# Optimization experiments

Measured on AMD Instinct MI355X. Metric: run time of the kernel, lower is better.

Reference implementation:

```python
import jax, jax.numpy as jnp
import numpy as np

N_EMBEDDINGS = 1024
EMBEDDING_DIM = 256
DECAY = 0.99
EPSILON = 1e-05


def setup_inputs() -> dict:
    key = jax.random.key(0)
    k1, k2, k3 = jax.random.split(key, 3)
    inputs = jax.random.normal(k1, (16, 64, 64, EMBEDDING_DIM), dtype=jnp.float32)
    codebook = jax.random.normal(k2, (N_EMBEDDINGS, EMBEDDING_DIM), dtype=jnp.float32)
    ema_w = jax.random.normal(k3, (N_EMBEDDINGS, EMBEDDING_DIM), dtype=jnp.float32)
    ema_cluster_size = jnp.zeros((N_EMBEDDINGS,), dtype=jnp.float32)
    return {"inputs": inputs, "codebook": codebook, "ema_w": ema_w,
            "ema_cluster_size": ema_cluster_size}


def reference(inputs, codebook, ema_w, ema_cluster_size):
    input_shape = inputs.shape
    flat = inputs.reshape(-1, EMBEDDING_DIM)  # [N, D]
    # Squared Euclidean pairwise distances: [N, K]
    dists = (jnp.sum(flat * flat, axis=1, keepdims=True)
             + jnp.sum(codebook * codebook, axis=1)[None, :]
             - 2.0 * flat @ codebook.T)
    idx = jnp.argmin(dists, axis=1)  # [N]
    encodings = jax.nn.one_hot(idx, N_EMBEDDINGS, dtype=flat.dtype)  # [N, K]
    quantized = (encodings @ codebook).reshape(input_shape)
    # EMA updates (training mode)
    cs = ema_cluster_size * DECAY + (1.0 - DECAY) * jnp.sum(encodings, axis=0)
    n = jnp.sum(cs)
    cs = (cs + EPSILON) / (n + cs * EPSILON) * n  # faithful to original expression
    dw = encodings.T @ flat  # [K, D] scatter-accumulate via matmul
    new_ema_w = ema_w * DECAY + (1.0 - DECAY) * dw
    new_codebook = new_ema_w / cs[:, None]
    return quantized, encodings, cs, new_ema_w, new_codebook
```

## Files before the change

### kernel.cpp

```cpp
#include <hip/hip_runtime.h>

#define N_ROWS 65536
#define D 256
#define K 1024
#define DECAYF 0.99f
#define OMDF 0.01f
#define EPSF 1e-5f

typedef _Float16 f16;
typedef _Float16 f16x8 __attribute__((ext_vector_type(8)));
typedef float f32x16 __attribute__((ext_vector_type(16)));

__global__ __launch_bounds__(256) void prep_kernel(const float* __restrict__ cb,
                                                   float* __restrict__ cnorm,
                                                   char* __restrict__ wsB,
                                                   float* __restrict__ dw,
                                                   float* __restrict__ counts) {
    const int tid = threadIdx.x;
    const int bid = blockIdx.x;
    const int g = bid * 256 + tid;
    *reinterpret_cast<float4*>(dw + (size_t)g * 4) = make_float4(0.f, 0.f, 0.f, 0.f);
    if (g < K) counts[g] = 0.f;
    {
        const int row = bid * 4 + (tid >> 6);
        const int lane = tid & 63;
        const float4 v = *reinterpret_cast<const float4*>(cb + (size_t)row * D + lane * 4);
        float s = v.x * v.x + v.y * v.y + v.z * v.z + v.w * v.w;
        #pragma unroll
        for (int m = 32; m; m >>= 1) s += __shfl_xor(s, m);
        if (lane == 0) cnorm[row] = s;
    }
    {
        const int sp = g & 15;
        const int c = (g >> 4) & 255;
        const int sd = g >> 12;
        const int ct = sd >> 2, dk = sd & 3;
        const int sl = sp ^ (c & 7);
        const int v = sl >> 3, ks = (sl >> 1) & 3, h = sl & 1;
        const float* src = cb + (size_t)(ct * 256 + c) * D + dk * 64 + ks * 16 + h * 8;
        f16 out[8];
        #pragma unroll
        for (int e = 0; e < 8; ++e) {
            const float f = src[e];
            const f16 hi = (f16)f;
            out[e] = v ? (f16)(f - (float)hi) : hi;
        }
        *reinterpret_cast<f16x8*>(wsB + (size_t)g * 16) = *reinterpret_cast<f16x8*>(out);
    }
}

__global__ __launch_bounds__(256, 2) void argmin_mfma_kernel(
        const float* __restrict__ x, const float* __restrict__ cb,
        const char* __restrict__ wsB, const float* __restrict__ cnorm,
        int* __restrict__ idx_out, float* __restrict__ counts,
        float* __restrict__ quant, float* __restrict__ enc) {
    __shared__ char smem[81920];
    char* Alds = smem;
    char* Blds = smem + 16384;
    const int tid = threadIdx.x;
    const int wave = tid >> 6;
    const int lane = tid & 63;
    const int rw = wave >> 1;
    const int cw = wave & 1;
    const int l31 = lane & 31;
    const int h = lane >> 5;
    const int n0 = blockIdx.x * 64;

    float bestv[16];
    int besti[16];
    #pragma unroll
    for (int r = 0; r < 16; ++r) { bestv[r] = 3.4e38f; besti[r] = 0; }

    const int s_row = tid >> 2;
    const int s_c4 = tid & 3;

    for (int ct = 0; ct < 4; ++ct) {
        f32x16 acc[4];
        #pragma unroll
        for (int cf = 0; cf < 4; ++cf)
            #pragma unroll
            for (int r = 0; r < 16; ++r) acc[cf][r] = 0.f;

        for (int dks = 0; dks < 4; ++dks) {
            const int dk = (ct & 1) ? (3 - dks) : dks;
            __syncthreads();
            if (!(ct > 0 && dks == 0)) {
                const float4* xs = reinterpret_cast<const float4*>(
                    x + (size_t)(n0 + s_row) * D + dk * 64 + s_c4 * 16);
                float f[16];
                {
                    const float4 f0 = xs[0], f1 = xs[1], f2 = xs[2], f3 = xs[3];
                    f[0]=f0.x; f[1]=f0.y; f[2]=f0.z; f[3]=f0.w;
                    f[4]=f1.x; f[5]=f1.y; f[6]=f1.z; f[7]=f1.w;
                    f[8]=f2.x; f[9]=f2.y; f[10]=f2.z; f[11]=f2.w;
                    f[12]=f3.x; f[13]=f3.y; f[14]=f3.z; f[15]=f3.w;
                }
                f16 hi[16], lo[16];
                #pragma unroll
                for (int e = 0; e < 16; ++e) {
                    hi[e] = (f16)f[e];
                    lo[e] = (f16)(f[e] - (float)hi[e]);
                }
                const int sw = s_row & 7;
                char* Abase = Alds + s_row * 256;
                *reinterpret_cast<f16x8*>(Abase + (((s_c4 * 2 + 0) ^ sw) * 16)) = *reinterpret_cast<f16x8*>(&hi[0]);
                *reinterpret_cast<f16x8*>(Abase + (((s_c4 * 2 + 1) ^ sw) * 16)) = *reinterpret_cast<f16x8*>(&hi[8]);
                *reinterpret_cast<f16x8*>(Abase + (((8 + s_c4 * 2 + 0) ^ sw) * 16)) = *reinterpret_cast<f16x8*>(&lo[0]);
                *reinterpret_cast<f16x8*>(Abase + (((8 + s_c4 * 2 + 1) ^ sw) * 16)) = *reinterpret_cast<f16x8*>(&lo[8]);
            }
            {
                const int4* gsrc = reinterpret_cast<const int4*>(wsB + ((size_t)(ct * 4 + dk) << 16));
                int4* ldst = reinterpret_cast<int4*>(Blds);
                #pragma unroll
                for (int i = 0; i < 16; ++i) ldst[tid + i * 256] = gsrc[tid + i * 256];
            }
            __syncthreads();
            const int arow = rw * 32 + l31;
            const int asw = arow & 7;
            #pragma unroll
            for (int ks = 0; ks < 4; ++ks) {
                const int sA = ks * 2 + h;
                const f16x8 Ah = *reinterpret_cast<const f16x8*>(Alds + arow * 256 + ((sA ^ asw) * 16));
                const f16x8 Al = *reinterpret_cast<const f16x8*>(Alds + arow * 256 + (((8 + sA) ^ asw) * 16));
                #pragma unroll
                for (int cf = 0; cf < 4; ++cf) {
                    const int bcode = cw * 128 + cf * 32 + l31;
                    const char* Bbase = Blds + bcode * 256;
                    const int bsw = bcode & 7;
                    const f16x8 Bh = *reinterpret_cast<const f16x8*>(Bbase + ((sA ^ bsw) * 16));
                    const f16x8 Bl = *reinterpret_cast<const f16x8*>(Bbase + (((8 + sA) ^ bsw) * 16));
                    acc[cf] = __builtin_amdgcn_mfma_f32_32x32x16_f16(Ah, Bh, acc[cf], 0, 0, 0);
                    acc[cf] = __builtin_amdgcn_mfma_f32_32x32x16_f16(Ah, Bl, acc[cf], 0, 0, 0);
                    acc[cf] = __builtin_amdgcn_mfma_f32_32x32x16_f16(Al, Bh, acc[cf], 0, 0, 0);
                }
            }
        }
        #pragma unroll
        for (int cf = 0; cf < 4; ++cf) {
            const int code = ct * 256 + cw * 128 + cf * 32 + l31;
            const float cn = cnorm[code];
            #pragma unroll
            for (int r = 0; r < 16; ++r) {
                const float dist = cn - 2.f * acc[cf][r];
                if (dist < bestv[r]) { bestv[r] = dist; besti[r] = code; }
            }
        }
    }
    #pragma unroll
    for (int r = 0; r < 16; ++r) {
        float v = bestv[r];
        int b = besti[r];
        #pragma unroll
        for (int m = 16; m; m >>= 1) {
            const float ov = __shfl_xor(v, m);
            const int ob = __shfl_xor(b, m);
            if (ov < v || (ov == v && ob < b)) { v = ov; b = ob; }
        }
        bestv[r] = v; besti[r] = b;
    }
    __syncthreads();
    float* Sv = reinterpret_cast<float*>(smem);
    int*   Si = reinterpret_cast<int*>(smem + 512);
    if (l31 == 0) {
        #pragma unroll
        for (int r = 0; r < 16; ++r) {
            const int row = rw * 32 + (r & 3) + 8 * (r >> 2) + 4 * h;
            Sv[cw * 64 + row] = bestv[r];
            Si[cw * 64 + row] = besti[r];
        }
    }
    __syncthreads();
    if (tid < 64) {
        const float v0 = Sv[tid], v1 = Sv[64 + tid];
        const int b0 = Si[tid], b1 = Si[64 + tid];
        const bool take1 = (v1 < v0) || (v1 == v0 && b1 < b0);
        const int b = take1 ? b1 : b0;
        idx_out[n0 + tid] = b;
        atomicAdd(&counts[b], 1.0f);
        Si[tid] = b;
    }
    __syncthreads();
    {
        const int k0 = tid * 4;
        #pragma unroll 4
        for (int r = 0; r < 64; ++r) {
            const int ir = Si[r];
            float4 v;
            v.x = (k0 == ir) ? 1.f : 0.f;
            v.y = (k0 + 1 == ir) ? 1.f : 0.f;
            v.z = (k0 + 2 == ir) ? 1.f : 0.f;
            v.w = (k0 + 3 == ir) ? 1.f : 0.f;
            *reinterpret_cast<float4*>(enc + (((size_t)(n0 + r)) << 10) + k0) = v;
        }
    }
    #pragma unroll
    for (int it = 0; it < 16; ++it) {
        const int r = it * 4 + wave;
        const int ir = Si[r];
        const float4 c = *reinterpret_cast<const float4*>(cb + (size_t)ir * D + lane * 4);
        *reinterpret_cast<float4*>(quant + (size_t)(n0 + r) * D + lane * 4) = c;
    }
}

__global__ __launch_bounds__(1024) void cs_scan_kernel(const float* __restrict__ ema_cs,
                                                       const float* __restrict__ counts,
                                                       float* __restrict__ cs_out,
                                                       int* __restrict__ cursor) {
    __shared__ float wsum[16];
    __shared__ int wisum[16];
    __shared__ float n_sh;
    const int k = threadIdx.x;
    const int wid = k >> 6;
    const int lane = k & 63;
    const float cnt = counts[k];
    const float c = ema_cs[k] * DECAYF + OMDF * cnt;
    const int ic = (int)cnt;
    int v = ic;
    #pragma unroll
    for (int d = 1; d < 64; d <<= 1) {
        const int t = __shfl_up(v, d);
        if (lane >= d) v += t;
    }
    float s = c;
    #pragma unroll
    for (int m = 32; m; m >>= 1) s += __shfl_xor(s, m);
    if (lane == 63) wisum[wid] = v;
    if (lane == 0) wsum[wid] = s;
    __syncthreads();
    if (k == 0) {
        float n = 0.f;
        for (int w = 0; w < 16; ++w) n += wsum[w];
        n_sh = n;
    }
    if (wid == 0 && lane < 16) {
        int wv = wisum[lane];
        #pragma unroll
        for (int d = 1; d < 16; d <<= 1) {
            const int t = __shfl_up(wv, d);
            if (lane >= d) wv += t;
        }
        wisum[lane] = wv;
    }
    __syncthreads();
    const float n = n_sh;
    cs_out[k] = (c + EPSF) / (n + c * EPSF) * n;
    const int wbase = (wid == 0) ? 0 : wisum[wid - 1];
    cursor[k] = wbase + v - ic;
}

__global__ __launch_bounds__(256) void scatter_kernel(const int* __restrict__ idx,
                                                      int* __restrict__ cursor,
                                                      int* __restrict__ rowlist,
                                                      int* __restrict__ codelist) {
    const int n = blockIdx.x * 256 + threadIdx.x;
    const int i = idx[n];
    const int pos = atomicAdd(&cursor[i], 1);
    rowlist[pos] = n;
    codelist[pos] = i;
}

__global__ __launch_bounds__(256) void chunk_sum_kernel(const float* __restrict__ x,
                                                        const int* __restrict__ rowlist,
                                                        const int* __restrict__ codelist,
                                                        float* __restrict__ dw) {
    const int wave = threadIdx.x >> 6;
    const int lane = threadIdx.x & 63;
    const int p0 = blockIdx.x * 32 + wave * 8;
    int rows[8], codes[8];
    #pragma unroll
    for (int j = 0; j < 8; ++j) {
        rows[j] = rowlist[p0 + j];
        codes[j] = codelist[p0 + j];
    }
    float4 v[8];
    #pragma unroll
    for (int j = 0; j < 8; ++j)
        v[j] = *reinterpret_cast<const float4*>(x + (size_t)rows[j] * D + lane * 4);
    float4 s = v[0];
    int cur = codes[0];
    #pragma unroll
    for (int j = 1; j < 8; ++j) {
        if (codes[j] != cur) {
            float* dst = dw + (size_t)cur * D + lane * 4;
            atomicAdd(dst + 0, s.x); atomicAdd(dst + 1, s.y);
            atomicAdd(dst + 2, s.z); atomicAdd(dst + 3, s.w);
            cur = codes[j];
            s = v[j];
        } else {
            s.x += v[j].x; s.y += v[j].y; s.z += v[j].z; s.w += v[j].w;
        }
    }
    float* dst = dw + (size_t)cur * D + lane * 4;
    atomicAdd(dst + 0, s.x); atomicAdd(dst + 1, s.y);
    atomicAdd(dst + 2, s.z); atomicAdd(dst + 3, s.w);
}

__global__ __launch_bounds__(256) void ema_kernel(const float* __restrict__ ema_w,
                                                  const float* __restrict__ dw,
                                                  const float* __restrict__ cs,
                                                  float* __restrict__ w_out,
                                                  float* __restrict__ cb_out) {
    const int e4 = blockIdx.x * blockDim.x + threadIdx.x;
    const int k = e4 >> 6;
    const float csk = cs[k];
    const float4 w = *reinterpret_cast<const float4*>(ema_w + (size_t)e4 * 4);
    const float4 d = *reinterpret_cast<const float4*>(dw + (size_t)e4 * 4);
    float4 nw, nc;
    nw.x = w.x * DECAYF + OMDF * d.x;
    nw.y = w.y * DECAYF + OMDF * d.y;
    nw.z = w.z * DECAYF + OMDF * d.z;
    nw.w = w.w * DECAYF + OMDF * d.w;
    nc.x = nw.x / csk; nc.y = nw.y / csk; nc.z = nw.z / csk; nc.w = nw.w / csk;
    *reinterpret_cast<float4*>(w_out + (size_t)e4 * 4) = nw;
    *reinterpret_cast<float4*>(cb_out + (size_t)e4 * 4) = nc;
}

extern "C" void kernel_launch(void* const* d_in, const int* in_sizes, int n_in,
                              void* d_out, int out_size, void* d_ws, size_t ws_size,
                              hipStream_t stream) {
    (void)in_sizes; (void)n_in; (void)out_size; (void)ws_size;
    const float* x      = (const float*)d_in[0];
    const float* cb     = (const float*)d_in[1];
    const float* ema_w  = (const float*)d_in[2];
    const float* ema_cs = (const float*)d_in[3];

    float* out    = (float*)d_out;
    float* quant  = out;
    float* enc    = quant + 16777216;
    float* cs_out = enc + 67108864;
    float* w_out  = cs_out + 1024;
    float* cb_out = w_out + 262144;

    float* ws       = (float*)d_ws;
    float* counts   = ws;
    float* dw       = ws + 1024;
    float* cnorm    = ws + 263168;
    int*   cursor   = (int*)(ws + 264192);
    int*   idx      = (int*)(ws + 265216);
    int*   rowlist  = (int*)(ws + 330752);
    int*   codelist = (int*)(ws + 396288);
    char*  wsB      = (char*)(ws + 461824);

    prep_kernel<<<256, 256, 0, stream>>>(cb, cnorm, wsB, dw, counts);
    argmin_mfma_kernel<<<N_ROWS / 64, 256, 0, stream>>>(x, cb, wsB, cnorm, idx, counts,
                                                        quant, enc);
    cs_scan_kernel<<<1, 1024, 0, stream>>>(ema_cs, counts, cs_out, cursor);
    scatter_kernel<<<N_ROWS / 256, 256, 0, stream>>>(idx, cursor, rowlist, codelist);
    chunk_sum_kernel<<<2048, 256, 0, stream>>>(x, rowlist, codelist, dw);
    ema_kernel<<<65536 / 256, 256, 0, stream>>>(ema_w, dw, cs_out, w_out, cb_out);
}
```

Before: 347.5 us.

## Split one-hot and quantized writes into separate nontemporal kernels, widen LDS swizzle

Moves writing the 256MB one-hot encoding matrix and the quantized output out of the MFMA argmin kernel into two dedicated streaming kernels that use nontemporal stores. The aim is to stop the compute kernel from stalling on the large write tail and to let the writes run at full bandwidth across the whole GPU. It also widens the LDS XOR swizzle from 8 to 16 slots to reduce bank conflicts. The split adds two kernel launches, and the new kernels must re-read the index array.

```diff
diff --git a/kernel.cpp b/kernel.cpp
--- a/kernel.cpp
+++ b/kernel.cpp
@@ -10,6 +10,7 @@
 typedef _Float16 f16;
 typedef _Float16 f16x8 __attribute__((ext_vector_type(8)));
 typedef float f32x16 __attribute__((ext_vector_type(16)));
+typedef float f32x4 __attribute__((ext_vector_type(4)));
 
 __global__ __launch_bounds__(256) void prep_kernel(const float* __restrict__ cb,
                                                    float* __restrict__ cnorm,
@@ -35,7 +36,7 @@
         const int c = (g >> 4) & 255;
         const int sd = g >> 12;
         const int ct = sd >> 2, dk = sd & 3;
-        const int sl = sp ^ (c & 7);
+        const int sl = sp ^ (c & 15);
         const int v = sl >> 3, ks = (sl >> 1) & 3, h = sl & 1;
         const float* src = cb + (size_t)(ct * 256 + c) * D + dk * 64 + ks * 16 + h * 8;
         f16 out[8];
@@ -50,10 +51,9 @@
 }
 
 __global__ __launch_bounds__(256, 2) void argmin_mfma_kernel(
-        const float* __restrict__ x, const float* __restrict__ cb,
-        const char* __restrict__ wsB, const float* __restrict__ cnorm,
-        int* __restrict__ idx_out, float* __restrict__ counts,
-        float* __restrict__ quant, float* __restrict__ enc) {
+        const float* __restrict__ x, const char* __restrict__ wsB,
+        const float* __restrict__ cnorm, int* __restrict__ idx_out,
+        float* __restrict__ counts) {
     __shared__ char smem[81920];
     char* Alds = smem;
     char* Blds = smem + 16384;
@@ -101,7 +101,7 @@
                     hi[e] = (f16)f[e];
                     lo[e] = (f16)(f[e] - (float)hi[e]);
                 }
-                const int sw = s_row & 7;
+                const int sw = s_row & 15;
                 char* Abase = Alds + s_row * 256;
                 *reinterpret_cast<f16x8*>(Abase + (((s_c4 * 2 + 0) ^ sw) * 16)) = *reinterpret_cast<f16x8*>(&hi[0]);
                 *reinterpret_cast<f16x8*>(Abase + (((s_c4 * 2 + 1) ^ sw) * 16)) = *reinterpret_cast<f16x8*>(&hi[8]);
@@ -116,7 +116,7 @@
             }
             __syncthreads();
             const int arow = rw * 32 + l31;
-            const int asw = arow & 7;
+            const int asw = arow & 15;
             #pragma unroll
             for (int ks = 0; ks < 4; ++ks) {
                 const int sA = ks * 2 + h;
@@ -126,7 +126,7 @@
                 for (int cf = 0; cf < 4; ++cf) {
                     const int bcode = cw * 128 + cf * 32 + l31;
                     const char* Bbase = Blds + bcode * 256;
-                    const int bsw = bcode & 7;
+                    const int bsw = bcode & 15;
                     const f16x8 Bh = *reinterpret_cast<const f16x8*>(Bbase + ((sA ^ bsw) * 16));
                     const f16x8 Bl = *reinterpret_cast<const f16x8*>(Bbase + (((8 + sA) ^ bsw) * 16));
                     acc[cf] = __builtin_amdgcn_mfma_f32_32x32x16_f16(Ah, Bh, acc[cf], 0, 0, 0);
@@ -177,28 +177,33 @@
         const int b = take1 ? b1 : b0;
         idx_out[n0 + tid] = b;
         atomicAdd(&counts[b], 1.0f);
-        Si[tid] = b;
-    }
-    __syncthreads();
-    {
-        const int k0 = tid * 4;
-        #pragma unroll 4
-        for (int r = 0; r < 64; ++r) {
-            const int ir = Si[r];
-            float4 v;
-            v.x = (k0 == ir) ? 1.f : 0.f;
-            v.y = (k0 + 1 == ir) ? 1.f : 0.f;
-            v.z = (k0 + 2 == ir) ? 1.f : 0.f;
-            v.w = (k0 + 3 == ir) ? 1.f : 0.f;
-            *reinterpret_cast<float4*>(enc + (((size_t)(n0 + r)) << 10) + k0) = v;
-        }
-    }
-    #pragma unroll
-    for (int it = 0; it < 16; ++it) {
-        const int r = it * 4 + wave;
-        const int ir = Si[r];
-        const float4 c = *reinterpret_cast<const float4*>(cb + (size_t)ir * D + lane * 4);
-        *reinterpret_cast<float4*>(quant + (size_t)(n0 + r) * D + lane * 4) = c;
+    }
+}
+
+__global__ __launch_bounds__(256) void quant_kernel(const float* __restrict__ cb,
+                                                    const int* __restrict__ idx,
+                                                    float* __restrict__ quant) {
+    const int n = blockIdx.x * 4 + (threadIdx.x >> 6);
+    const int lane = threadIdx.x & 63;
+    const int i = idx[n];
+    const f32x4 c = *reinterpret_cast<const f32x4*>(cb + (size_t)i * D + lane * 4);
+    __builtin_nontemporal_store(c, reinterpret_cast<f32x4*>(quant + (size_t)n * D + lane * 4));
+}
+
+__global__ __launch_bounds__(256) void enc_kernel(const int* __restrict__ idx,
+                                                  float* __restrict__ enc) {
+    const int total = N_ROWS * (K / 4);
+    for (int g = blockIdx.x * blockDim.x + threadIdx.x; g < total;
+         g += gridDim.x * blockDim.x) {
+        const int n = g >> 8;
+        const int k0 = (g & 255) * 4;
+        const int i = idx[n];
+        f32x4 v;
+        v[0] = (k0 == i) ? 1.f : 0.f;
+        v[1] = (k0 + 1 == i) ? 1.f : 0.f;
+        v[2] = (k0 + 2 == i) ? 1.f : 0.f;
+        v[3] = (k0 + 3 == i) ? 1.f : 0.f;
+        __builtin_nontemporal_store(v, reinterpret_cast<f32x4*>(enc + (size_t)g * 4));
     }
 }
 
@@ -342,8 +347,9 @@
     char*  wsB      = (char*)(ws + 461824);
 
     prep_kernel<<<256, 256, 0, stream>>>(cb, cnorm, wsB, dw, counts);
-    argmin_mfma_kernel<<<N_ROWS / 64, 256, 0, stream>>>(x, cb, wsB, cnorm, idx, counts,
-                                                        quant, enc);
+    argmin_mfma_kernel<<<N_ROWS / 64, 256, 0, stream>>>(x, wsB, cnorm, idx, counts);
+    quant_kernel<<<N_ROWS / 4, 256, 0, stream>>>(cb, idx, quant);
+    enc_kernel<<<2048, 256, 0, stream>>>(idx, enc);
     cs_scan_kernel<<<1, 1024, 0, stream>>>(ema_cs, counts, cs_out, cursor);
     scatter_kernel<<<N_ROWS / 256, 256, 0, stream>>>(idx, cursor, rowlist, codelist);
     chunk_sum_kernel<<<2048, 256, 0, stream>>>(x, rowlist, codelist, dw);
```

Result: faster. 336.1 us (-3.3%).
